# Kernel tuning notes

Hardware: AMD Instinct MI355X
Metric: run time of the kernel (lower is better)

Reference implementation:

```python
import math
import jax, jax.numpy as jnp
import numpy as np

B, L, ENC_IN, D_MODEL, D_FF, E_LAYERS, N_HEADS, FACTOR = 4, 2048, 32, 512, 2048, 2, 8, 5


def layer_norm(x, g, b, eps=1e-5):
    mu = jnp.mean(x, axis=-1, keepdims=True)
    var = jnp.mean((x - mu) ** 2, axis=-1, keepdims=True)
    return (x - mu) / jnp.sqrt(var + eps) * g + b


def positional_encoding(length, d_model):
    pos = np.arange(length, dtype=np.float32)[:, None]
    div = np.exp(np.arange(0, d_model, 2, dtype=np.float32) * -(math.log(10000.0) / d_model))
    pe = np.zeros((length, d_model), dtype=np.float32)
    pe[:, 0::2] = np.sin(pos * div)
    pe[:, 1::2] = np.cos(pos * div)
    return jnp.asarray(pe)


def circ_conv1d(x, w, b=None):
    # x: [B,L,Cin], w: [Cout,Cin,3]; kernel 3, circular padding 1, stride 1 -> [B,L,Cout]
    xc = jnp.transpose(x, (0, 2, 1))
    xc = jnp.pad(xc, ((0, 0), (0, 0), (1, 1)), mode='wrap')
    y = jax.lax.conv_general_dilated(xc, w, (1,), 'VALID',
                                     dimension_numbers=('NCH', 'OIH', 'NCH'))
    if b is not None:
        y = y + b[None, :, None]
    return jnp.transpose(y, (0, 2, 1))


def prob_attention(Q, K, V, key):
    # Q,K,V: [B,H,L,D]; ProbAttention(mask_flag=False, factor=5)
    Bq, H, Lq, D = Q.shape
    sample_k = min(FACTOR * int(math.ceil(math.log(Lq))), Lq)  # U_part
    n_top = min(FACTOR * int(math.ceil(math.log(Lq))), Lq)    # u
    idx = jax.random.randint(key, (Lq, sample_k), 0, Lq)
    K_samp = K[:, :, idx, :]                                  # [B,H,L,sample_k,D]
    QK_samp = jnp.einsum('bhld,bhlud->bhlu', Q, K_samp)
    M = QK_samp.max(axis=-1) - QK_samp.sum(axis=-1) / Lq      # sparsity measure [B,H,L]
    _, M_top = jax.lax.top_k(M, n_top)                        # [B,H,u]
    Q_red = jnp.take_along_axis(Q, M_top[..., None], axis=2)  # [B,H,u,D]
    scores = jnp.einsum('bhud,bhkd->bhuk', Q_red, K) / math.sqrt(D)
    attn = jax.nn.softmax(scores, axis=-1)
    upd = jnp.einsum('bhuk,bhkd->bhud', attn, V)
    # initial context = mean of V (mask_flag=False), overwritten at top-u rows
    ctx = jnp.broadcast_to(jnp.mean(V, axis=2, keepdims=True), (Bq, H, Lq, D))
    bi = jnp.arange(Bq)[:, None, None]
    hi = jnp.arange(H)[None, :, None]
    return ctx.at[bi, hi, M_top].set(upd)


def attention_layer(x, Wq, bq, Wk, bk, Wv, bv, Wo, bo, key):
    Bx, Lx, dm = x.shape
    D = dm // N_HEADS
    def split(h):
        return h.reshape(Bx, Lx, N_HEADS, D).transpose(0, 2, 1, 3)
    q = split(x @ Wq.T + bq)
    k = split(x @ Wk.T + bk)
    v = split(x @ Wv.T + bv)
    ctx = prob_attention(q, k, v, key)
    ctx = ctx.transpose(0, 2, 1, 3).reshape(Bx, Lx, dm)
    return ctx @ Wo.T + bo


def encoder_layer(x, Wq, bq, Wk, bk, Wv, bv, Wo, bo, W1, b1, W2, b2, g1, be1, g2, be2, key):
    x = x + attention_layer(x, Wq, bq, Wk, bk, Wv, bv, Wo, bo, key)
    x = layer_norm(x, g1, be1)
    y = jax.nn.gelu(x @ W1.T + b1, approximate=False)  # conv1 (kernel 1) + gelu
    y = y @ W2.T + b2                                  # conv2 (kernel 1)
    return layer_norm(x + y, g2, be2)


def conv_distil(x, w, b, bn_g, bn_b):
    y = circ_conv1d(x, w, b)
    mu = jnp.mean(y, axis=(0, 1))                      # BatchNorm1d (training-mode stats)
    var = jnp.mean((y - mu) ** 2, axis=(0, 1))
    y = (y - mu) / jnp.sqrt(var + 1e-5) * bn_g + bn_b
    y = jax.nn.elu(y)
    yt = jnp.transpose(y, (0, 2, 1))                   # MaxPool1d(k=3, s=2, p=1)
    yt = jax.lax.reduce_window(yt, -jnp.inf, jax.lax.max,
                               (1, 1, 3), (1, 1, 2), [(0, 0), (0, 0), (1, 1)])
    return jnp.transpose(yt, (0, 2, 1))


def setup_inputs() -> dict:
    key = jax.random.key(0)
    ks = iter(jax.random.split(key, 32))
    def nrm(shape, sc=0.02):
        return jax.random.normal(next(ks), shape, jnp.float32) * sc
    return {
        'x_enc': jax.random.normal(next(ks), (B, L, ENC_IN), jnp.float32),
        'tok_w': nrm((D_MODEL, ENC_IN, 3), 0.1),
        'Wq': nrm((E_LAYERS, D_MODEL, D_MODEL)), 'bq': jnp.zeros((E_LAYERS, D_MODEL)),
        'Wk': nrm((E_LAYERS, D_MODEL, D_MODEL)), 'bk': jnp.zeros((E_LAYERS, D_MODEL)),
        'Wv': nrm((E_LAYERS, D_MODEL, D_MODEL)), 'bv': jnp.zeros((E_LAYERS, D_MODEL)),
        'Wo': nrm((E_LAYERS, D_MODEL, D_MODEL)), 'bo': jnp.zeros((E_LAYERS, D_MODEL)),
        'W1': nrm((E_LAYERS, D_FF, D_MODEL)), 'b1': jnp.zeros((E_LAYERS, D_FF)),
        'W2': nrm((E_LAYERS, D_MODEL, D_FF)), 'b2': jnp.zeros((E_LAYERS, D_MODEL)),
        'ln1_g': jnp.ones((E_LAYERS, D_MODEL)), 'ln1_b': jnp.zeros((E_LAYERS, D_MODEL)),
        'ln2_g': jnp.ones((E_LAYERS, D_MODEL)), 'ln2_b': jnp.zeros((E_LAYERS, D_MODEL)),
        'conv_w': nrm((D_MODEL, D_MODEL, 3)), 'conv_b': jnp.zeros((D_MODEL,)),
        'bn_g': jnp.ones((D_MODEL,)), 'bn_b': jnp.zeros((D_MODEL,)),
        'normf_g': jnp.ones((D_MODEL,)), 'normf_b': jnp.zeros((D_MODEL,)),
        'proj_w': nrm((ENC_IN, D_MODEL)), 'proj_b': jnp.zeros((ENC_IN,)),
    }


def reference(x_enc, tok_w, Wq, bq, Wk, bk, Wv, bv, Wo, bo, W1, b1, W2, b2,
              ln1_g, ln1_b, ln2_g, ln2_b, conv_w, conv_b, bn_g, bn_b,
              normf_g, normf_b, proj_w, proj_b):
    keys = jax.random.split(jax.random.key(42), E_LAYERS)
    # DataEmbedding: circular token conv (no bias) + sinusoidal positional embedding
    x = circ_conv1d(x_enc, tok_w) + positional_encoding(x_enc.shape[1], D_MODEL)[None]
    for i in range(E_LAYERS):
        x = encoder_layer(x, Wq[i], bq[i], Wk[i], bk[i], Wv[i], bv[i], Wo[i], bo[i],
                          W1[i], b1[i], W2[i], b2[i],
                          ln1_g[i], ln1_b[i], ln2_g[i], ln2_b[i], keys[i])
        if i == 0:  # single distillation ConvLayer after first encoder layer
            x = conv_distil(x, conv_w, conv_b, bn_g, bn_b)
    x = layer_norm(x, normf_g, normf_b)
    out = x @ proj_w.T + proj_b
    return out[:, :L]  # [:, :seq_len] slice (no-op after distillation halves length)
```

## Files before the change

### kernel.cpp

```cpp
#include <hip/hip_runtime.h>
#include <cstdint>
#include <cmath>


#define NB 4
#define DM 512
#define NH 8
#define HD 64
#define QS 1536

typedef unsigned short ushort_t;
typedef __bf16 bf16x8 __attribute__((ext_vector_type(8)));
typedef float floatx4 __attribute__((ext_vector_type(4)));
typedef unsigned short ushort8_t __attribute__((ext_vector_type(8)));

__device__ inline ushort_t f2b(float f) {
  uint32_t u = __float_as_uint(f);
  uint32_t r = (u + 0x7fffu + ((u >> 16) & 1u)) >> 16;
  return (ushort_t)r;
}
__device__ inline float b2f(ushort_t u) {
  return __uint_as_float((uint32_t)u << 16);
}

__global__ void castqkv_k(const float* __restrict__ Wq,
                          const float* __restrict__ Wk,
                          const float* __restrict__ Wv,
                          ushort_t* __restrict__ out) {
  int gid = blockIdx.x * 256 + threadIdx.x;
  if (gid >= 393216) return;
  int ly = gid / 196608, r4 = gid - ly * 196608;
  int r = r4 >> 7, c4 = r4 & 127;
  int sel = r >> 9, srow = r & 511;
  const float* src = (sel == 0 ? Wq : sel == 1 ? Wk : Wv) + ly * 262144 +
                     srow * 512 + c4 * 4;
  float4 v = *(const float4*)src;
  ushort4 o;
  o.x = f2b(v.x); o.y = f2b(v.y); o.z = f2b(v.z); o.w = f2b(v.w);
  ((ushort4*)out)[ly * 196608 + r * 128 + c4] = o;
}

__global__ void castw3_k(const float* __restrict__ Wo,
                         const float* __restrict__ W1,
                         const float* __restrict__ W2,
                         const float* __restrict__ tw,
                         ushort_t* __restrict__ oWo, ushort_t* __restrict__ oW1,
                         ushort_t* __restrict__ oW2, ushort_t* __restrict__ otw) {
  int gid = blockIdx.x * 256 + threadIdx.x;
  if (gid >= 1191936) return;
  const float* src;
  ushort4* dst;
  int i;
  if (gid < 131072) { src = Wo; dst = (ushort4*)oWo; i = gid; }
  else if (gid < 655360) { src = W1; dst = (ushort4*)oW1; i = gid - 131072; }
  else if (gid < 1179648) { src = W2; dst = (ushort4*)oW2; i = gid - 655360; }
  else { src = tw; dst = (ushort4*)otw; i = gid - 1179648; }
  float4 v = ((const float4*)src)[i];
  ushort4 o;
  o.x = f2b(v.x); o.y = f2b(v.y); o.z = f2b(v.z); o.w = f2b(v.w);
  dst[i] = o;
}

__global__ void castw_conv_k(const float* __restrict__ in,
                             ushort_t* __restrict__ out) {
  int gid = blockIdx.x * 256 + threadIdx.x;
  int d = gid / 1536, r = gid - d * 1536;
  int t = r >> 9, i = r & 511;
  out[gid] = f2b(in[d * 1536 + i * 3 + t]);
}

__global__ void castproj_k(const float* __restrict__ w,
                           float* __restrict__ wt) {
  int gid = blockIdx.x * 256 + threadIdx.x;
  int k = gid >> 5, n = gid & 31;
  wt[gid] = w[n * 512 + k];
}

__global__ void setup_small_k(const float* __restrict__ bq,
                              const float* __restrict__ bk,
                              const float* __restrict__ bv,
                              float* __restrict__ ZB,
                              float* __restrict__ BQKV) {
  int gid = blockIdx.x * 256 + threadIdx.x;
  if (gid >= 3584) return;
  if (gid < 512) { ZB[gid] = 0.f; return; }
  int g = gid - 512;
  int layer = g / 1536, r = g - layer * 1536;
  float v;
  if (r < 512) v = bq[layer * 512 + r];
  else if (r < 1024) v = bk[layer * 512 + r - 512];
  else v = bv[layer * 512 + r - 1024];
  BQKV[g] = v;
}

__host__ __device__ inline void threefry2x32(uint32_t k0, uint32_t k1,
                                             uint32_t c0, uint32_t c1,
                                             uint32_t* o0, uint32_t* o1) {
  uint32_t ks0 = k0, ks1 = k1, ks2 = k0 ^ k1 ^ 0x1BD11BDAu;
  uint32_t x0 = c0 + ks0;
  uint32_t x1 = c1 + ks1;
  const uint32_t rotA[4] = {13u, 15u, 26u, 6u};
  const uint32_t rotB[4] = {17u, 29u, 16u, 24u};
  uint32_t ks[3] = {ks0, ks1, ks2};
  #pragma unroll
  for (int i = 0; i < 5; ++i) {
    const uint32_t* r = (i & 1) ? rotB : rotA;
    #pragma unroll
    for (int j = 0; j < 4; ++j) {
      x0 += x1;
      x1 = (x1 << r[j]) | (x1 >> (32u - r[j]));
      x1 ^= x0;
    }
    x0 += ks[(i + 1) % 3];
    x1 += ks[(i + 2) % 3] + (uint32_t)(i + 1);
  }
  *o0 = x0; *o1 = x1;
}

__global__ void gen_idx_k(int* __restrict__ idx, int n, int mask,
                          uint32_t k0, uint32_t k1) {
  int i = blockIdx.x * 256 + threadIdx.x;
  if (i < n) {
    uint32_t o0, o1;
    threefry2x32(k0, k1, 0u, (uint32_t)i, &o0, &o1);
    idx[i] = (int)((o0 ^ o1) & (uint32_t)mask);
  }
}

__device__ inline float wave_sum64(float v) {
  #pragma unroll
  for (int o = 32; o > 0; o >>= 1) v += __shfl_xor(v, o, 64);
  return v;
}

__global__ void pe_k(float* __restrict__ pe) {
  int i = blockIdx.x * 256 + threadIdx.x;
  int d = i & 511, l = i >> 9;
  int j2 = d & ~1;
  float div = expf((float)j2 * -1.7988946039e-2f);
  float ang = (float)l * div;
  pe[i] = (d & 1) ? cosf(ang) : sinf(ang);
}

__global__ void im2col_tok_k(const float* __restrict__ xe,
                             ushort_t* __restrict__ A) {
  int gid = blockIdx.x * 256 + threadIdx.x;
  int col = gid % 96;
  int row = gid / 96;
  int c = col / 3, t = col - c * 3;
  int b = row >> 11, l = row & 2047;
  int ls = (l + t - 1) & 2047;
  A[gid] = f2b(xe[((size_t)b * 2048 + ls) * 32 + c]);
}

__device__ inline void gload16(const ushort_t* g, ushort_t* l) {
  __builtin_amdgcn_global_load_lds(
      (const __attribute__((address_space(1))) unsigned int*)(const void*)g,
      (__attribute__((address_space(3))) unsigned int*)(void*)l, 16, 0, 0);
}

template <int TM, int CONV, int GELU, int OMODE, int ADDPE>
__global__ __launch_bounds__(512, 4) void mgemm_k(
    const ushort_t* __restrict__ A, const ushort_t* __restrict__ W,
    const float* __restrict__ bias, float* __restrict__ Cf,
    ushort_t* __restrict__ Cb, const float* __restrict__ pe,
    int X, int ldc, int K) {
  constexpr int MT = TM / 64;
  constexpr int AG = TM / 128;
  constexpr int BUFSZ = (TM + 128) * 32;
  constexpr int SHSZ = (2 * BUFSZ > 18432) ? 2 * BUFSZ : 18432;
  __shared__ __align__(16) ushort_t SH[SHSZ];
  int id = blockIdx.x;
  int cc = id & 7, j = id >> 3;
  int bx = j % X;
  int by = (j / X) * 8 + cc;
  int m0 = by * TM, n0 = bx * 128;
  int t = threadIdx.x;
  int lane = t & 63, wv = t >> 6;
  int rl = lane >> 2, cl = (lane & 3) * 8;
  int RaA = wv * (16 * AG);
  int RaB = wv * 16;
  const ushort_t* gA[AG];
  int cbv[AG], clrv[AG], lAoff[AG];
  #pragma unroll
  for (int g = 0; g < AG; ++g) {
    int ar = m0 + RaA + g * 16 + rl;
    gA[g] = A + (size_t)ar * K + cl;
    cbv[g] = ar >> 11;
    clrv[g] = ar & 2047;
    lAoff[g] = (RaA + g * 16) * 32;
  }
  const ushort_t* gB = W + (size_t)(n0 + RaB + rl) * K + cl;
  int lBoff = TM * 32 + RaB * 32;

  int quad = lane >> 4, lr = lane & 15;
  int wm = wv >> 1, wn = wv & 1;

  floatx4 acc[MT][4] = {};
  #pragma unroll
  for (int g = 0; g < AG; ++g) {
    if (CONV) {
      int ls = (clrv[g] - 1) & 2047;
      gload16(A + ((size_t)(cbv[g] * 2048 + ls) * 512 + cl), SH + lAoff[g]);
    } else {
      gload16(gA[g], SH + lAoff[g]);
    }
  }
  gload16(gB, SH + lBoff);
  __syncthreads();
  int cur = 0;
  for (int ks = 0; ks < K; ks += 32) {
    int nxt = ks + 32;
    if (nxt < K) {
      int bb = (cur ^ 1) * BUFSZ;
      #pragma unroll
      for (int g = 0; g < AG; ++g) {
        if (CONV) {
          int tt = nxt >> 9;
          int c = (nxt & 511) + cl;
          int ls = (clrv[g] + tt - 1) & 2047;
          gload16(A + ((size_t)(cbv[g] * 2048 + ls) * 512 + c),
                  SH + bb + lAoff[g]);
        } else {
          gload16(gA[g] + nxt, SH + bb + lAoff[g]);
        }
      }
      gload16(gB + nxt, SH + bb + lBoff);
    }
    const ushort_t* Ab = SH + cur * BUFSZ;
    const ushort_t* Bb = Ab + TM * 32;
    bf16x8 av[MT], bv[4];
    #pragma unroll
    for (int mt = 0; mt < MT; ++mt)
      av[mt] =
          *(const bf16x8*)&Ab[(wm * (16 * MT) + mt * 16 + lr) * 32 + quad * 8];
    #pragma unroll
    for (int nt = 0; nt < 4; ++nt)
      bv[nt] = *(const bf16x8*)&Bb[(wn * 64 + nt * 16 + lr) * 32 + quad * 8];
    #pragma unroll
    for (int mt = 0; mt < MT; ++mt)
      #pragma unroll
      for (int nt = 0; nt < 4; ++nt)
        acc[mt][nt] = __builtin_amdgcn_mfma_f32_16x16x32_bf16(
            av[mt], bv[nt], acc[mt][nt], 0, 0, 0);
    __syncthreads();
    cur ^= 1;
  }

  if (OMODE == 0) {
    #pragma unroll
    for (int nt = 0; nt < 4; ++nt) {
      int col = n0 + wn * 64 + nt * 16 + lr;
      float bsv = bias[col];
      #pragma unroll
      for (int mt = 0; mt < MT; ++mt) {
        int row0 = m0 + wm * (16 * MT) + mt * 16 + quad * 4;
        #pragma unroll
        for (int r = 0; r < 4; ++r) {
          int row = row0 + r;
          float v = acc[mt][nt][r] + bsv;
          if (ADDPE) v += pe[(size_t)(row & 2047) * ldc + col];
          if (GELU) v = 0.5f * v * (1.0f + erff(v * 0.70710678118654752f));
          Cf[(size_t)row * ldc + col] = v;
        }
      }
    }
  } else {
    ushort_t* ep = SH + wv * 2304;
    #pragma unroll
    for (int p = 0; p < MT / 2; ++p) {
      #pragma unroll
      for (int nt = 0; nt < 4; ++nt) {
        int col = n0 + wn * 64 + nt * 16 + lr;
        float bsv = bias[col];
        #pragma unroll
        for (int ml = 0; ml < 2; ++ml) {
          int mt = p * 2 + ml;
          #pragma unroll
          for (int r = 0; r < 4; ++r) {
            int row = m0 + wm * (16 * MT) + mt * 16 + quad * 4 + r;
            float v = acc[mt][nt][r] + bsv;
            if (ADDPE) v += pe[(size_t)(row & 2047) * ldc + col];
            if (GELU) v = 0.5f * v * (1.0f + erff(v * 0.70710678118654752f));
            if (OMODE == 2) Cf[(size_t)row * ldc + col] = v;
            ep[(ml * 16 + quad * 4 + r) * 72 + nt * 16 + lr] = f2b(v);
          }
        }
      }
      int r8 = lane >> 3, c8 = (lane & 7) * 8;
      #pragma unroll
      for (int i = 0; i < 4; ++i) {
        int row = i * 8 + r8;
        ushort8_t vv = *(const ushort8_t*)&ep[row * 72 + c8];
        *(ushort8_t*)&Cb[(size_t)(m0 + wm * (16 * MT) + p * 32 + row) * ldc +
                         n0 + wn * 64 + c8] = vv;
      }
    }
  }
}

__global__ __launch_bounds__(256) void proj_k(
    const float* __restrict__ A, const float* __restrict__ Wt,
    const float* __restrict__ bias, float* __restrict__ C) {
  int t = threadIdx.x;
  int n = t & 31, ml = t >> 5;
  int m = blockIdx.x * 8 + ml;
  const float* a = A + (size_t)m * DM;
  float a0 = 0.f, a1 = 0.f, a2 = 0.f, a3 = 0.f;
  #pragma unroll 4
  for (int k = 0; k < DM; k += 4) {
    float4 av = *(const float4*)&a[k];
    a0 += av.x * Wt[k * 32 + n];
    a1 += av.y * Wt[(k + 1) * 32 + n];
    a2 += av.z * Wt[(k + 2) * 32 + n];
    a3 += av.w * Wt[(k + 3) * 32 + n];
  }
  C[(size_t)m * 32 + n] = (a0 + a2) + (a1 + a3) + bias[n];
}

__global__ __launch_bounds__(128) void ln_k(
    const float* __restrict__ A, const float* __restrict__ Bres,
    const float* __restrict__ g, const float* __restrict__ be,
    float* __restrict__ O, ushort_t* __restrict__ Ob) {
  int r = blockIdx.x, t = threadIdx.x;
  __shared__ float lds[2];
  float4 v = ((const float4*)(A + (size_t)r * DM))[t];
  if (Bres) {
    float4 u = ((const float4*)(Bres + (size_t)r * DM))[t];
    v.x += u.x; v.y += u.y; v.z += u.z; v.w += u.w;
  }
  float s = wave_sum64(v.x + v.y + v.z + v.w);
  int w = t >> 6;
  if ((t & 63) == 0) lds[w] = s;
  __syncthreads();
  float mu = (lds[0] + lds[1]) * (1.0f / 512.0f);
  __syncthreads();
  float dx = v.x - mu, dy = v.y - mu, dz = v.z - mu, dw = v.w - mu;
  float sq = wave_sum64(dx * dx + dy * dy + dz * dz + dw * dw);
  if ((t & 63) == 0) lds[w] = sq;
  __syncthreads();
  float var = (lds[0] + lds[1]) * (1.0f / 512.0f);
  float inv = 1.0f / sqrtf(var + 1e-5f);
  float4 gv = ((const float4*)g)[t];
  float4 bv = ((const float4*)be)[t];
  float4 o;
  o.x = dx * inv * gv.x + bv.x;
  o.y = dy * inv * gv.y + bv.y;
  o.z = dz * inv * gv.z + bv.z;
  o.w = dw * inv * gv.w + bv.w;
  ((float4*)(O + (size_t)r * DM))[t] = o;
  if (Ob) {
    ushort4 ob;
    ob.x = f2b(o.x); ob.y = f2b(o.y); ob.z = f2b(o.z); ob.w = f2b(o.w);
    ((ushort4*)(Ob + (size_t)r * DM))[t] = ob;
  }
}

template <int UU>
__global__ __launch_bounds__(256) void qk_m_k(
    const ushort_t* __restrict__ QKVb, const int* __restrict__ idx,
    float* __restrict__ Mout, int Lx) {
  int l = blockIdx.x;
  int b = threadIdx.x >> 6;
  int lane = threadIdx.x & 63;
  const ushort_t* qp = QKVb + ((size_t)b * Lx + l) * QS + lane * 8;
  float q[8];
  {
    ushort8_t qv = *(const ushort8_t*)qp;
    #pragma unroll
    for (int c = 0; c < 8; ++c) q[c] = b2f(qv[c]);
  }
  const ushort_t* Kbase = QKVb + (size_t)b * Lx * QS + 512 + lane * 8;
  const int* ip = idx + (size_t)l * UU;
  float maxv = -INFINITY, sumv = 0.f;
  #pragma unroll
  for (int u0 = 0; u0 < UU; u0 += 8) {
    ushort8_t kv[8];
    #pragma unroll
    for (int j = 0; j < 8; ++j) {
      if (u0 + j < UU)
        kv[j] = *(const ushort8_t*)(Kbase + (size_t)ip[u0 + j] * QS);
    }
    #pragma unroll
    for (int j = 0; j < 8; ++j) {
      if (u0 + j < UU) {
        float p = 0.f;
        #pragma unroll
        for (int c = 0; c < 8; ++c) p += q[c] * b2f(kv[j][c]);
        p += __shfl_xor(p, 1, 64);
        p += __shfl_xor(p, 2, 64);
        p += __shfl_xor(p, 4, 64);
        maxv = fmaxf(maxv, p);
        sumv += p;
      }
    }
  }
  if ((lane & 7) == 0) {
    int h = lane >> 3;
    Mout[(size_t)(b * 8 + h) * Lx + l] = maxv - sumv / (float)Lx;
  }
}

__global__ __launch_bounds__(1024) void topk_k(
    const float* __restrict__ Mbuf, int* __restrict__ Mtop, int Lx, int U) {
  int nch = Lx >> 8;
  int bh = blockIdx.x / nch, ch = blockIdx.x % nch;
  const float* m = Mbuf + (size_t)bh * Lx;
  __shared__ float sm[2048];
  __shared__ int part[1024];
  int t = threadIdx.x;
  int c = t & 255, q = t >> 8;
  for (int i = t; i < Lx; i += 1024) sm[i] = m[i];
  __syncthreads();
  int i0 = (ch << 8) + c;
  float v0 = sm[i0];
  int r0 = 0;
  int qlen = Lx >> 2;
  int j0 = q * qlen, j1 = j0 + qlen;
  for (int j = j0; j < j1; j += 4) {
    float4 mj = *(const float4*)&sm[j];
    r0 += (mj.x > v0) || (mj.x == v0 && (j + 0) < i0);
    r0 += (mj.y > v0) || (mj.y == v0 && (j + 1) < i0);
    r0 += (mj.z > v0) || (mj.z == v0 && (j + 2) < i0);
    r0 += (mj.w > v0) || (mj.w == v0 && (j + 3) < i0);
  }
  part[t] = r0;
  __syncthreads();
  if (q == 0) {
    int r = part[c] + part[c + 256] + part[c + 512] + part[c + 768];
    if (r < U) Mtop[bh * U + r] = i0;
  }
}

__global__ __launch_bounds__(512) void meanv1_k(const ushort_t* __restrict__ QKVb,
                                                float* __restrict__ part,
                                                int Lx) {
  int b = blockIdx.x >> 4, chunk = blockIdx.x & 15;
  int rows = Lx >> 4;
  int t = threadIdx.x;
  const ushort_t* vp =
      QKVb + ((size_t)b * Lx + (size_t)chunk * rows) * QS + 1024 + t;
  float s = 0.f;
  for (int l = 0; l < rows; ++l) s += b2f(vp[(size_t)l * QS]);
  part[(size_t)blockIdx.x * DM + t] = s;
}
__global__ __launch_bounds__(512) void meanv2_k(const float* __restrict__ part,
                                                float* __restrict__ mv,
                                                int Lx) {
  int b = blockIdx.x, t = threadIdx.x;
  float s = 0.f;
  #pragma unroll
  for (int c = 0; c < 16; ++c) s += part[(size_t)(b * 16 + c) * DM + t];
  mv[b * DM + t] = s / (float)Lx;
}

__global__ void fillctx_k(ushort_t* __restrict__ ctx,
                          const float* __restrict__ mv, int Lx) {
  size_t i4 = (size_t)blockIdx.x * 256 + threadIdx.x;
  int col4 = (int)(i4 & 127);
  size_t row = i4 >> 7;
  int b = (int)(row / (size_t)Lx);
  const float* m = mv + b * DM + col4 * 4;
  ushort4 o;
  o.x = f2b(m[0]); o.y = f2b(m[1]); o.z = f2b(m[2]); o.w = f2b(m[3]);
  ((ushort4*)ctx)[i4] = o;
}

template <int UP>
__global__ __launch_bounds__(256) void attn_mfma_k(
    const ushort_t* __restrict__ QKVb, const int* __restrict__ Mtop,
    float* __restrict__ part, int Lx, int U, int nblk) {
  __shared__ ushort_t Ps[4][UP * 72];
  __shared__ ushort_t Vs[4][64 * 64];
  int bh = blockIdx.x / nblk, blkc = blockIdx.x % nblk;
  int h = bh & 7, b = bh >> 3;
  int t = threadIdx.x;
  int wv = t >> 6, lane = t & 63;
  int quad = lane >> 4, lr = lane & 15;
  int chunk = blkc * 4 + wv;
  int k0 = chunk * 64;
  const ushort_t* Qb = QKVb + (size_t)b * Lx * QS + h * HD;
  const ushort_t* Kb = Qb + 512;
  const ushort_t* Vb = Qb + 1024;

  bf16x8 qf[3][2];
  #pragma unroll
  for (int mt = 0; mt < 3; ++mt) {
    int u = mt * 16 + lr;
    int qi = Mtop[bh * U + (u < U ? u : U - 1)];
    const ushort_t* qp = Qb + (size_t)qi * QS + quad * 8;
    qf[mt][0] = *(const bf16x8*)qp;
    qf[mt][1] = *(const bf16x8*)(qp + 32);
  }

  ushort_t* vs = Vs[wv];
  #pragma unroll
  for (int i = 0; i < 8; ++i) {
    int cid = i * 64 + lane;
    int k = cid >> 3, c = cid & 7;
    ushort8_t v = *(const ushort8_t*)(Vb + (size_t)(k0 + k) * QS + c * 8);
    *(ushort8_t*)&vs[k * 64 + ((c * 8) ^ (((k >> 3) & 3) << 4))] = v;
  }

  floatx4 Sa[3][4] = {};
  #pragma unroll
  for (int kt = 0; kt < 4; ++kt) {
    const ushort_t* kp = Kb + (size_t)(k0 + kt * 16 + lr) * QS + quad * 8;
    bf16x8 kf0 = *(const bf16x8*)kp;
    bf16x8 kf1 = *(const bf16x8*)(kp + 32);
    #pragma unroll
    for (int mt = 0; mt < 3; ++mt) {
      Sa[mt][kt] = __builtin_amdgcn_mfma_f32_16x16x32_bf16(
          qf[mt][0], kf0, Sa[mt][kt], 0, 0, 0);
      Sa[mt][kt] = __builtin_amdgcn_mfma_f32_16x16x32_bf16(
          qf[mt][1], kf1, Sa[mt][kt], 0, 0, 0);
    }
  }

  float m_[3][4], l_[3][4];
  #pragma unroll
  for (int mt = 0; mt < 3; ++mt) {
    #pragma unroll
    for (int kt = 0; kt < 4; ++kt) Sa[mt][kt] *= 0.125f;
    #pragma unroll
    for (int r = 0; r < 4; ++r) {
      float mx = fmaxf(fmaxf(Sa[mt][0][r], Sa[mt][1][r]),
                       fmaxf(Sa[mt][2][r], Sa[mt][3][r]));
      #pragma unroll
      for (int o = 1; o <= 8; o <<= 1) mx = fmaxf(mx, __shfl_xor(mx, o, 64));
      float rs = 0.f;
      #pragma unroll
      for (int kt = 0; kt < 4; ++kt) {
        float e = __expf(Sa[mt][kt][r] - mx);
        Sa[mt][kt][r] = e;
        rs += e;
      }
      #pragma unroll
      for (int o = 1; o <= 8; o <<= 1) rs += __shfl_xor(rs, o, 64);
      m_[mt][r] = mx;
      l_[mt][r] = rs;
    }
  }

  ushort_t* ps = Ps[wv];
  floatx4 Oa[3][4] = {};
  #pragma unroll
  for (int pass = 0; pass < 2; ++pass) {
    #pragma unroll
    for (int mt = 0; mt < 3; ++mt)
      #pragma unroll
      for (int kt = 0; kt < 4; ++kt)
        #pragma unroll
        for (int r = 0; r < 4; ++r) {
          float e = Sa[mt][kt][r];
          ushort_t hb = f2b(e);
          ps[(mt * 16 + quad * 4 + r) * 72 + kt * 16 + lr] = hb;
          Sa[mt][kt][r] = e - b2f(hb);
        }
    #pragma unroll
    for (int kk = 0; kk < 2; ++kk) {
      bf16x8 pf[3];
      #pragma unroll
      for (int mt = 0; mt < 3; ++mt)
        pf[mt] = *(const bf16x8*)&ps[(mt * 16 + lr) * 72 + kk * 32 + quad * 8];
      #pragma unroll
      for (int nt = 0; nt < 4; ++nt) {
        ushort8_t vt;
        #pragma unroll
        for (int j = 0; j < 8; ++j)
          vt[j] = vs[(kk * 32 + quad * 8 + j) * 64 +
                     ((nt * 16 + lr) ^ (quad << 4))];
        bf16x8 vf = *(bf16x8*)&vt;
        #pragma unroll
        for (int mt = 0; mt < 3; ++mt)
          Oa[mt][nt] = __builtin_amdgcn_mfma_f32_16x16x32_bf16(
              pf[mt], vf, Oa[mt][nt], 0, 0, 0);
      }
    }
  }

  float* pb = part + (size_t)(bh * (nblk * 4) + chunk) * U * 66;
  #pragma unroll
  for (int mt = 0; mt < 3; ++mt) {
    #pragma unroll
    for (int r = 0; r < 4; ++r) {
      int u = mt * 16 + quad * 4 + r;
      if (u < U) {
        #pragma unroll
        for (int nt = 0; nt < 4; ++nt)
          pb[(size_t)u * 66 + nt * 16 + lr] = Oa[mt][nt][r];
        if (lr == 0) {
          pb[(size_t)u * 66 + 64] = m_[mt][r];
          pb[(size_t)u * 66 + 65] = l_[mt][r];
        }
      }
    }
  }
}

__global__ __launch_bounds__(64) void attn_merge_k(
    const float* __restrict__ part, const int* __restrict__ Mtop,
    ushort_t* __restrict__ ctx, int Lx, int U, int nchunk) {
  int bu = blockIdx.x;
  int u = bu % U, bh = bu / U;
  int h = bh & 7, b = bh >> 3;
  int d = threadIdx.x;
  float M = -INFINITY;
  for (int c = 0; c < nchunk; ++c)
    M = fmaxf(M, part[((size_t)(bh * nchunk + c) * U + u) * 66 + 64]);
  float L = 0.f, O = 0.f;
  for (int c = 0; c < nchunk; ++c) {
    const float* pp = part + ((size_t)(bh * nchunk + c) * U + u) * 66;
    float w = __expf(pp[64] - M);
    L += pp[65] * w;
    O += pp[d] * w;
  }
  int qi = Mtop[bh * U + u];
  ctx[((size_t)b * Lx + qi) * DM + h * HD + d] = f2b(O / L);
}

__global__ __launch_bounds__(256) void bn1_k(const float* __restrict__ Y,
                                             float* __restrict__ ps,
                                             float* __restrict__ pq) {
  int blk = blockIdx.x;
  int t = threadIdx.x;
  float s0 = 0, q0 = 0, s1 = 0, q1 = 0;
  const float* base = Y + (size_t)blk * 256 * DM;
  for (int r = 0; r < 256; ++r) {
    float a = base[(size_t)r * DM + t];
    float b = base[(size_t)r * DM + t + 256];
    s0 += a; q0 += a * a; s1 += b; q1 += b * b;
  }
  ps[blk * DM + t] = s0; ps[blk * DM + t + 256] = s1;
  pq[blk * DM + t] = q0; pq[blk * DM + t + 256] = q1;
}
__global__ __launch_bounds__(512) void bn2_k(const float* __restrict__ ps,
                                             const float* __restrict__ pq,
                                             float* __restrict__ mu,
                                             float* __restrict__ var) {
  int t = threadIdx.x;
  float s = 0, q = 0;
  #pragma unroll
  for (int c = 0; c < 32; ++c) { s += ps[c * DM + t]; q += pq[c * DM + t]; }
  float m = s * (1.0f / 8192.f);
  mu[t] = m;
  var[t] = q * (1.0f / 8192.f) - m * m;
}

__global__ void bnpool_k(const float* __restrict__ Y,
                         const float* __restrict__ mu,
                         const float* __restrict__ var,
                         const float* __restrict__ g,
                         const float* __restrict__ be, float* __restrict__ O,
                         ushort_t* __restrict__ Ob) {
  size_t i = (size_t)blockIdx.x * 256 + threadIdx.x;
  int c = (int)(i & 511);
  size_t row = i >> 9;
  int lo = (int)(row & 1023);
  int b = (int)(row >> 10);
  float sc = g[c] / sqrtf(var[c] + 1e-5f);
  float sh = be[c] - mu[c] * sc;
  int l0 = 2 * lo - 1;
  float m = -INFINITY;
  #pragma unroll
  for (int tt = 0; tt < 3; ++tt) {
    int l = l0 + tt;
    if (l >= 0 && l < 2048) {
      float v = Y[((size_t)b * 2048 + l) * DM + c] * sc + sh;
      v = v > 0.f ? v : expm1f(v);
      m = fmaxf(m, v);
    }
  }
  O[i] = m;
  Ob[i] = f2b(m);
}

extern "C" void kernel_launch(void* const* d_in, const int* in_sizes, int n_in,
                              void* d_out, int out_size, void* d_ws,
                              size_t ws_size, hipStream_t stream) {
  (void)in_sizes; (void)n_in; (void)out_size; (void)ws_size;
  const float* x_enc  = (const float*)d_in[0];
  const float* tok_w  = (const float*)d_in[1];
  const float* Wq     = (const float*)d_in[2];
  const float* bq     = (const float*)d_in[3];
  const float* Wk     = (const float*)d_in[4];
  const float* bk     = (const float*)d_in[5];
  const float* Wv     = (const float*)d_in[6];
  const float* bv     = (const float*)d_in[7];
  const float* Wo     = (const float*)d_in[8];
  const float* bo     = (const float*)d_in[9];
  const float* W1     = (const float*)d_in[10];
  const float* b1     = (const float*)d_in[11];
  const float* W2     = (const float*)d_in[12];
  const float* b2     = (const float*)d_in[13];
  const float* ln1_g  = (const float*)d_in[14];
  const float* ln1_b  = (const float*)d_in[15];
  const float* ln2_g  = (const float*)d_in[16];
  const float* ln2_b  = (const float*)d_in[17];
  const float* conv_w = (const float*)d_in[18];
  const float* conv_b = (const float*)d_in[19];
  const float* bn_g   = (const float*)d_in[20];
  const float* bn_b   = (const float*)d_in[21];
  const float* normf_g = (const float*)d_in[22];
  const float* normf_b = (const float*)d_in[23];
  const float* proj_w = (const float*)d_in[24];
  const float* proj_b = (const float*)d_in[25];
  float* out = (float*)d_out;
  float* ws = (float*)d_ws;

  float* X    = ws;
  float* SCR  = ws + 4194304;
  ushort_t* CTXb = (ushort_t*)(ws + 16777216);
  float* Y2   = ws + 20971520;
  float* Mb   = ws + 25165824;
  float* MV   = ws + 25231360;
  float* MVP  = ws + 25233408;
  float* BNps = ws + 25266176;
  float* BNpq = ws + 25282560;
  float* BNmu = ws + 25298944;
  float* BNvr = ws + 25299456;
  float* ZB   = ws + 25299968;
  float* BQKV = ws + 25300480;
  int*   IDX  = (int*)(ws + 25303552);
  int*   MT   = (int*)(ws + 25385472);
  ushort_t* U0   = (ushort_t*)(ws + 25386752);
  ushort_t* Xb   = U0;
  ushort_t* Hb   = U0 + 4194304;
  ushort_t* QKVb = Hb;
  ushort_t* Wqkvb= U0 + 20971520;
  ushort_t* Wob  = U0 + 22544384;
  ushort_t* W1b  = U0 + 23068672;
  ushort_t* W2b  = U0 + 25165824;
  ushort_t* Cwb  = U0 + 27262976;
  ushort_t* Twb  = U0 + 28049408;
  ushort_t* Atok = U0 + 28098560;
  float* PEf = ws + 39829248;
  float* PWt = ws + 40877824;

  castqkv_k<<<1536, 256, 0, stream>>>(Wq, Wk, Wv, Wqkvb);
  castw3_k<<<4656, 256, 0, stream>>>(Wo, W1, W2, tok_w, Wob, W1b, W2b, Twb);
  castw_conv_k<<<3072, 256, 0, stream>>>(conv_w, Cwb);
  castproj_k<<<64, 256, 0, stream>>>(proj_w, PWt);
  setup_small_k<<<14, 256, 0, stream>>>(bq, bk, bv, ZB, BQKV);
  pe_k<<<4096, 256, 0, stream>>>(PEf);
  im2col_tok_k<<<3072, 256, 0, stream>>>(x_enc, Atok);

  mgemm_k<128, 0, 0, 2, 1><<<256, 512, 0, stream>>>(
      Atok, Twb, ZB, X, Xb, PEf, 4, DM, 96);

  for (int layer = 0; layer < 2; ++layer) {
    const int Lx = (layer == 0) ? 2048 : 1024;
    const int U  = (layer == 0) ? 40 : 35;
    const int M  = NB * Lx;
    const int Yt = M / 128;
    const int Y2t = M / 256;
    const int NCHT = Lx / 64;
    const int NBLK = NCHT / 4;

    uint32_t kl0, kl1, s0, s1;
    threefry2x32(0u, 42u, 0u, (uint32_t)layer, &kl0, &kl1);
    threefry2x32(kl0, kl1, 0u, 1u, &s0, &s1);
    int nidx = Lx * U;
    gen_idx_k<<<(nidx + 255) / 256, 256, 0, stream>>>(IDX, nidx, Lx - 1, s0, s1);

    mgemm_k<256, 0, 0, 1, 0><<<12 * Y2t, 512, 0, stream>>>(
        Xb, Wqkvb + (size_t)layer * 786432, BQKV + layer * 1536, nullptr, QKVb,
        nullptr, 12, QS, DM);

    if (layer == 0)
      qk_m_k<40><<<Lx, 256, 0, stream>>>(QKVb, IDX, Mb, Lx);
    else
      qk_m_k<35><<<Lx, 256, 0, stream>>>(QKVb, IDX, Mb, Lx);
    topk_k<<<NB * NH * (Lx >> 8), 1024, 0, stream>>>(Mb, MT, Lx, U);
    meanv1_k<<<NB * 16, 512, 0, stream>>>(QKVb, MVP, Lx);
    meanv2_k<<<NB, 512, 0, stream>>>(MVP, MV, Lx);
    fillctx_k<<<(M * DM / 4) / 256, 256, 0, stream>>>(CTXb, MV, Lx);
    attn_mfma_k<48><<<NB * NH * NBLK, 256, 0, stream>>>(QKVb, MT, Y2, Lx, U,
                                                        NBLK);
    attn_merge_k<<<NB * NH * U, 64, 0, stream>>>(Y2, MT, CTXb, Lx, U, NCHT);

    mgemm_k<128, 0, 0, 0, 0><<<4 * Yt, 512, 0, stream>>>(
        CTXb, Wob + (size_t)layer * 262144, bo + layer * DM, Y2, nullptr,
        nullptr, 4, DM, DM);
    ln_k<<<M, 128, 0, stream>>>(X, Y2, ln1_g + layer * DM, ln1_b + layer * DM, X, Xb);

    mgemm_k<256, 0, 1, 1, 0><<<16 * Y2t, 512, 0, stream>>>(
        Xb, W1b + (size_t)layer * 1048576, b1 + layer * 2048, nullptr, Hb,
        nullptr, 16, 2048, DM);
    mgemm_k<128, 0, 0, 0, 0><<<4 * Yt, 512, 0, stream>>>(
        Hb, W2b + (size_t)layer * 1048576, b2 + layer * DM, Y2, nullptr,
        nullptr, 4, DM, 2048);
    ln_k<<<M, 128, 0, stream>>>(X, Y2, ln2_g + layer * DM, ln2_b + layer * DM, X, Xb);

    if (layer == 0) {
      mgemm_k<128, 1, 0, 0, 0><<<4 * 64, 512, 0, stream>>>(
          Xb, Cwb, conv_b, Y2, nullptr, nullptr, 4, DM, 1536);
      bn1_k<<<32, 256, 0, stream>>>(Y2, BNps, BNpq);
      bn2_k<<<1, 512, 0, stream>>>(BNps, BNpq, BNmu, BNvr);
      bnpool_k<<<(NB * 1024 * 512) / 256, 256, 0, stream>>>(
          Y2, BNmu, BNvr, bn_g, bn_b, X, Xb);
    }
  }

  ln_k<<<NB * 1024, 128, 0, stream>>>(X, nullptr, normf_g, normf_b, SCR, nullptr);
  proj_k<<<512, 256, 0, stream>>>(SCR, PWt, proj_b, out);
}
```

Measured before the change: 626.7 us.

## Split-K the N=512 GEMMs and fold partial sums into layernorm/batchnorm consumers

Adds a SPLITK template mode that launches two grid halves, each covering half of K, and writes the partial fp32 results to two separate buffers. The residual layernorm, BN statistics and BN-pool kernels now add both partials plus the bias. This is meant to double the block count for the narrow Wo, W2 and distil-conv GEMMs so more CUs are busy. It also moves the QKV and W1 GEMMs from 256-row to 128-row tiles for more blocks. The cost is extra fp32 partial-buffer traffic on both the write and the read side.

```diff
diff --git a/kernel.cpp b/kernel.cpp
--- a/kernel.cpp
+++ b/kernel.cpp
@@ -159,18 +159,25 @@
       (__attribute__((address_space(3))) unsigned int*)(void*)l, 16, 0, 0);
 }
 
-template <int TM, int CONV, int GELU, int OMODE, int ADDPE>
+template <int TM, int CONV, int GELU, int OMODE, int ADDPE, int SPLITK>
 __global__ __launch_bounds__(512, 4) void mgemm_k(
     const ushort_t* __restrict__ A, const ushort_t* __restrict__ W,
     const float* __restrict__ bias, float* __restrict__ Cf,
-    ushort_t* __restrict__ Cb, const float* __restrict__ pe,
-    int X, int ldc, int K) {
+    float* __restrict__ Cf2, ushort_t* __restrict__ Cb,
+    const float* __restrict__ pe, int X, int ldc, int K) {
   constexpr int MT = TM / 64;
   constexpr int AG = TM / 128;
   constexpr int BUFSZ = (TM + 128) * 32;
   constexpr int SHSZ = (2 * BUFSZ > 18432) ? 2 * BUFSZ : 18432;
   __shared__ __align__(16) ushort_t SH[SHSZ];
   int id = blockIdx.x;
+  int half = 0;
+  if (SPLITK == 2) {
+    int nb = gridDim.x >> 1;
+    if (id >= nb) { half = 1; id -= nb; }
+  }
+  int kbase = half * (K >> 1);
+  int KK = (SPLITK == 2) ? (K >> 1) : K;
   int cc = id & 7, j = id >> 3;
   int bx = j % X;
   int by = (j / X) * 8 + cc;
@@ -185,12 +192,12 @@
   #pragma unroll
   for (int g = 0; g < AG; ++g) {
     int ar = m0 + RaA + g * 16 + rl;
-    gA[g] = A + (size_t)ar * K + cl;
+    gA[g] = A + (size_t)ar * K + kbase + cl;
     cbv[g] = ar >> 11;
     clrv[g] = ar & 2047;
     lAoff[g] = (RaA + g * 16) * 32;
   }
-  const ushort_t* gB = W + (size_t)(n0 + RaB + rl) * K + cl;
+  const ushort_t* gB = W + (size_t)(n0 + RaB + rl) * K + kbase + cl;
   int lBoff = TM * 32 + RaB * 32;
 
   int quad = lane >> 4, lr = lane & 15;
@@ -200,8 +207,11 @@
   #pragma unroll
   for (int g = 0; g < AG; ++g) {
     if (CONV) {
-      int ls = (clrv[g] - 1) & 2047;
-      gload16(A + ((size_t)(cbv[g] * 2048 + ls) * 512 + cl), SH + lAoff[g]);
+      int kg = kbase;
+      int tt = kg >> 9;
+      int c = (kg & 511) + cl;
+      int ls = (clrv[g] + tt - 1) & 2047;
+      gload16(A + ((size_t)(cbv[g] * 2048 + ls) * 512 + c), SH + lAoff[g]);
     } else {
       gload16(gA[g], SH + lAoff[g]);
     }
@@ -209,15 +219,16 @@
   gload16(gB, SH + lBoff);
   __syncthreads();
   int cur = 0;
-  for (int ks = 0; ks < K; ks += 32) {
+  for (int ks = 0; ks < KK; ks += 32) {
     int nxt = ks + 32;
-    if (nxt < K) {
+    if (nxt < KK) {
       int bb = (cur ^ 1) * BUFSZ;
       #pragma unroll
       for (int g = 0; g < AG; ++g) {
         if (CONV) {
-          int tt = nxt >> 9;
-          int c = (nxt & 511) + cl;
+          int kg = kbase + nxt;
+          int tt = kg >> 9;
+          int c = (kg & 511) + cl;
           int ls = (clrv[g] + tt - 1) & 2047;
           gload16(A + ((size_t)(cbv[g] * 2048 + ls) * 512 + c),
                   SH + bb + lAoff[g]);
@@ -247,7 +258,20 @@
     cur ^= 1;
   }
 
-  if (OMODE == 0) {
+  if (SPLITK == 2) {
+    float* dst = half ? Cf2 : Cf;
+    #pragma unroll
+    for (int nt = 0; nt < 4; ++nt) {
+      int col = n0 + wn * 64 + nt * 16 + lr;
+      #pragma unroll
+      for (int mt = 0; mt < MT; ++mt) {
+        int row0 = m0 + wm * (16 * MT) + mt * 16 + quad * 4;
+        #pragma unroll
+        for (int r = 0; r < 4; ++r)
+          dst[(size_t)(row0 + r) * ldc + col] = acc[mt][nt][r];
+      }
+    }
+  } else if (OMODE == 0) {
     #pragma unroll
     for (int nt = 0; nt < 4; ++nt) {
       int col = n0 + wn * 64 + nt * 16 + lr;
@@ -320,6 +344,7 @@
 
 __global__ __launch_bounds__(128) void ln_k(
     const float* __restrict__ A, const float* __restrict__ Bres,
+    const float* __restrict__ Bres2, const float* __restrict__ cbias,
     const float* __restrict__ g, const float* __restrict__ be,
     float* __restrict__ O, ushort_t* __restrict__ Ob) {
   int r = blockIdx.x, t = threadIdx.x;
@@ -327,6 +352,14 @@
   float4 v = ((const float4*)(A + (size_t)r * DM))[t];
   if (Bres) {
     float4 u = ((const float4*)(Bres + (size_t)r * DM))[t];
+    v.x += u.x; v.y += u.y; v.z += u.z; v.w += u.w;
+  }
+  if (Bres2) {
+    float4 u = ((const float4*)(Bres2 + (size_t)r * DM))[t];
+    v.x += u.x; v.y += u.y; v.z += u.z; v.w += u.w;
+  }
+  if (cbias) {
+    float4 u = ((const float4*)cbias)[t];
     v.x += u.x; v.y += u.y; v.z += u.z; v.w += u.w;
   }
   float s = wave_sum64(v.x + v.y + v.z + v.w);
@@ -619,16 +652,20 @@
   ctx[((size_t)b * Lx + qi) * DM + h * HD + d] = f2b(O / L);
 }
 
-__global__ __launch_bounds__(256) void bn1_k(const float* __restrict__ Y,
+__global__ __launch_bounds__(256) void bn1_k(const float* __restrict__ Y0,
+                                             const float* __restrict__ Y1,
+                                             const float* __restrict__ cb,
                                              float* __restrict__ ps,
                                              float* __restrict__ pq) {
   int blk = blockIdx.x;
   int t = threadIdx.x;
+  float cb0 = cb[t], cb1 = cb[t + 256];
   float s0 = 0, q0 = 0, s1 = 0, q1 = 0;
-  const float* base = Y + (size_t)blk * 256 * DM;
+  const float* b0 = Y0 + (size_t)blk * 256 * DM;
+  const float* b1 = Y1 + (size_t)blk * 256 * DM;
   for (int r = 0; r < 256; ++r) {
-    float a = base[(size_t)r * DM + t];
-    float b = base[(size_t)r * DM + t + 256];
+    float a = b0[(size_t)r * DM + t] + b1[(size_t)r * DM + t] + cb0;
+    float b = b0[(size_t)r * DM + t + 256] + b1[(size_t)r * DM + t + 256] + cb1;
     s0 += a; q0 += a * a; s1 += b; q1 += b * b;
   }
   ps[blk * DM + t] = s0; ps[blk * DM + t + 256] = s1;
@@ -647,7 +684,9 @@
   var[t] = q * (1.0f / 8192.f) - m * m;
 }
 
-__global__ void bnpool_k(const float* __restrict__ Y,
+__global__ void bnpool_k(const float* __restrict__ Y0,
+                         const float* __restrict__ Y1,
+                         const float* __restrict__ cb,
                          const float* __restrict__ mu,
                          const float* __restrict__ var,
                          const float* __restrict__ g,
@@ -660,13 +699,15 @@
   int b = (int)(row >> 10);
   float sc = g[c] / sqrtf(var[c] + 1e-5f);
   float sh = be[c] - mu[c] * sc;
+  float cbv = cb[c];
   int l0 = 2 * lo - 1;
   float m = -INFINITY;
   #pragma unroll
   for (int tt = 0; tt < 3; ++tt) {
     int l = l0 + tt;
     if (l >= 0 && l < 2048) {
-      float v = Y[((size_t)b * 2048 + l) * DM + c] * sc + sh;
+      size_t off = ((size_t)b * 2048 + l) * DM + c;
+      float v = (Y0[off] + Y1[off] + cbv) * sc + sh;
       v = v > 0.f ? v : expm1f(v);
       m = fmaxf(m, v);
     }
@@ -709,7 +750,8 @@
   float* ws = (float*)d_ws;
 
   float* X    = ws;
-  float* SCR  = ws + 4194304;
+  float* Y2B  = ws + 4194304;
+  float* SCR  = ws + 8388608;
   ushort_t* CTXb = (ushort_t*)(ws + 16777216);
   float* Y2   = ws + 20971520;
   float* Mb   = ws + 25165824;
@@ -745,15 +787,14 @@
   pe_k<<<4096, 256, 0, stream>>>(PEf);
   im2col_tok_k<<<3072, 256, 0, stream>>>(x_enc, Atok);
 
-  mgemm_k<128, 0, 0, 2, 1><<<256, 512, 0, stream>>>(
-      Atok, Twb, ZB, X, Xb, PEf, 4, DM, 96);
+  mgemm_k<128, 0, 0, 2, 1, 1><<<256, 512, 0, stream>>>(
+      Atok, Twb, ZB, X, nullptr, Xb, PEf, 4, DM, 96);
 
   for (int layer = 0; layer < 2; ++layer) {
     const int Lx = (layer == 0) ? 2048 : 1024;
     const int U  = (layer == 0) ? 40 : 35;
     const int M  = NB * Lx;
     const int Yt = M / 128;
-    const int Y2t = M / 256;
     const int NCHT = Lx / 64;
     const int NBLK = NCHT / 4;
 
@@ -763,9 +804,9 @@
     int nidx = Lx * U;
     gen_idx_k<<<(nidx + 255) / 256, 256, 0, stream>>>(IDX, nidx, Lx - 1, s0, s1);
 
-    mgemm_k<256, 0, 0, 1, 0><<<12 * Y2t, 512, 0, stream>>>(
-        Xb, Wqkvb + (size_t)layer * 786432, BQKV + layer * 1536, nullptr, QKVb,
-        nullptr, 12, QS, DM);
+    mgemm_k<128, 0, 0, 1, 0, 1><<<12 * Yt, 512, 0, stream>>>(
+        Xb, Wqkvb + (size_t)layer * 786432, BQKV + layer * 1536, nullptr,
+        nullptr, QKVb, nullptr, 12, QS, DM);
 
     if (layer == 0)
       qk_m_k<40><<<Lx, 256, 0, stream>>>(QKVb, IDX, Mb, Lx);
@@ -779,29 +820,32 @@
                                                         NBLK);
     attn_merge_k<<<NB * NH * U, 64, 0, stream>>>(Y2, MT, CTXb, Lx, U, NCHT);
 
-    mgemm_k<128, 0, 0, 0, 0><<<4 * Yt, 512, 0, stream>>>(
-        CTXb, Wob + (size_t)layer * 262144, bo + layer * DM, Y2, nullptr,
+    mgemm_k<128, 0, 0, 0, 0, 2><<<2 * 4 * Yt, 512, 0, stream>>>(
+        CTXb, Wob + (size_t)layer * 262144, nullptr, Y2, Y2B, nullptr,
         nullptr, 4, DM, DM);
-    ln_k<<<M, 128, 0, stream>>>(X, Y2, ln1_g + layer * DM, ln1_b + layer * DM, X, Xb);
-
-    mgemm_k<256, 0, 1, 1, 0><<<16 * Y2t, 512, 0, stream>>>(
-        Xb, W1b + (size_t)layer * 1048576, b1 + layer * 2048, nullptr, Hb,
-        nullptr, 16, 2048, DM);
-    mgemm_k<128, 0, 0, 0, 0><<<4 * Yt, 512, 0, stream>>>(
-        Hb, W2b + (size_t)layer * 1048576, b2 + layer * DM, Y2, nullptr,
+    ln_k<<<M, 128, 0, stream>>>(X, Y2, Y2B, bo + layer * DM,
+                                ln1_g + layer * DM, ln1_b + layer * DM, X, Xb);
+
+    mgemm_k<128, 0, 1, 1, 0, 1><<<16 * Yt, 512, 0, stream>>>(
+        Xb, W1b + (size_t)layer * 1048576, b1 + layer * 2048, nullptr, nullptr,
+        Hb, nullptr, 16, 2048, DM);
+    mgemm_k<128, 0, 0, 0, 0, 2><<<2 * 4 * Yt, 512, 0, stream>>>(
+        Hb, W2b + (size_t)layer * 1048576, nullptr, Y2, Y2B, nullptr,
         nullptr, 4, DM, 2048);
-    ln_k<<<M, 128, 0, stream>>>(X, Y2, ln2_g + layer * DM, ln2_b + layer * DM, X, Xb);
+    ln_k<<<M, 128, 0, stream>>>(X, Y2, Y2B, b2 + layer * DM,
+                                ln2_g + layer * DM, ln2_b + layer * DM, X, Xb);
 
     if (layer == 0) {
-      mgemm_k<128, 1, 0, 0, 0><<<4 * 64, 512, 0, stream>>>(
-          Xb, Cwb, conv_b, Y2, nullptr, nullptr, 4, DM, 1536);
-      bn1_k<<<32, 256, 0, stream>>>(Y2, BNps, BNpq);
+      mgemm_k<128, 1, 0, 0, 0, 2><<<2 * 4 * 64, 512, 0, stream>>>(
+          Xb, Cwb, nullptr, Y2, Y2B, nullptr, nullptr, 4, DM, 1536);
+      bn1_k<<<32, 256, 0, stream>>>(Y2, Y2B, conv_b, BNps, BNpq);
       bn2_k<<<1, 512, 0, stream>>>(BNps, BNpq, BNmu, BNvr);
       bnpool_k<<<(NB * 1024 * 512) / 256, 256, 0, stream>>>(
-          Y2, BNmu, BNvr, bn_g, bn_b, X, Xb);
-    }
-  }
-
-  ln_k<<<NB * 1024, 128, 0, stream>>>(X, nullptr, normf_g, normf_b, SCR, nullptr);
+          Y2, Y2B, conv_b, BNmu, BNvr, bn_g, bn_b, X, Xb);
+    }
+  }
+
+  ln_k<<<NB * 1024, 128, 0, stream>>>(X, nullptr, nullptr, nullptr, normf_g,
+                                      normf_b, SCR, nullptr);
   proj_k<<<512, 256, 0, stream>>>(SCR, PWt, proj_b, out);
 }
```

Result: no change. 618.3 us (-1.3%).
